# Kernel tuning notes

Hardware: AMD Instinct MI355X
Metric: run time of the kernel (lower is better)

Reference implementation:

```python
import jax, jax.numpy as jnp
import numpy as np

D_IN = 32
D_MODEL = 128
B, T = 512, 512
INPUT_DIM = 2 * D_IN  # concat_mask=True, d_u=0


def setup_inputs() -> dict:
    key = jax.random.key(0)
    ks = jax.random.split(key, 8)
    scale = 0.05
    return {
        "x": jax.random.normal(ks[0], (B, T, D_IN), dtype=jnp.float32),
        "W_ih": jax.random.normal(ks[1], (3 * D_MODEL, INPUT_DIM), dtype=jnp.float32) * scale,
        "W_hh": jax.random.normal(ks[2], (3 * D_MODEL, D_MODEL), dtype=jnp.float32) * scale,
        "b_ih": jax.random.normal(ks[3], (3 * D_MODEL,), dtype=jnp.float32) * scale,
        "b_hh": jax.random.normal(ks[4], (3 * D_MODEL,), dtype=jnp.float32) * scale,
        "W_out": jax.random.normal(ks[5], (D_IN, D_MODEL), dtype=jnp.float32) * scale,
        "b_out": jax.random.normal(ks[6], (D_IN,), dtype=jnp.float32) * scale,
        "mask": jax.random.randint(ks[7], (B, T, D_IN), 0, 2, dtype=jnp.int32),
    }


def reference(x, W_ih, W_hh, b_ih, b_hh, W_out, b_out, mask):
    m_bool = mask.astype(bool)                      # [B,T,d_in]
    m_f = mask.astype(x.dtype)
    x = jnp.where(m_bool, x, jnp.zeros_like(x))     # zero-fill missing

    h0 = jnp.zeros((x.shape[0], D_MODEL), dtype=x.dtype)   # state_init='zero'
    x_hat0 = h0 @ W_out.T + b_out                   # readout of initial state

    def gru_cell(x_t, h):
        gx = x_t @ W_ih.T + b_ih                    # [B, 3*d_model]
        gh = h @ W_hh.T + b_hh
        xr, xz, xn = jnp.split(gx, 3, axis=-1)
        hr, hz, hn = jnp.split(gh, 3, axis=-1)
        r = jax.nn.sigmoid(xr + hr)
        z = jax.nn.sigmoid(xz + hz)
        n = jnp.tanh(xn + r * hn)
        return (1.0 - z) * n + z * h

    def step(carry, inp):
        h, x_hat = carry
        x_s, mb_s, mf_s = inp                       # [B,d_in] each
        x_p = jnp.where(mb_s, x_s, x_hat)           # fill blanks with prediction
        x_t = jnp.concatenate([x_p, mf_s], axis=-1) # concat_mask=True
        h_new = gru_cell(x_t, h)
        x_hat_new = h_new @ W_out.T + b_out
        return (h_new, x_hat_new), x_hat_new

    # scan over steps 0..T-2 (time-major)
    xs = jnp.swapaxes(x[:, :-1], 0, 1)              # [T-1, B, d_in]
    mbs = jnp.swapaxes(m_bool[:, :-1], 0, 1)
    mfs = jnp.swapaxes(m_f[:, :-1], 0, 1)
    _, preds = jax.lax.scan(step, (h0, x_hat0), (xs, mbs, mfs))  # [T-1, B, d_in]

    out = jnp.concatenate([x_hat0[None], preds], axis=0)         # [T, B, d_in]
    return jnp.swapaxes(out, 0, 1)                                # [B, T, d_in]
```

## Files before the change

### kernel.cpp

```cpp
#include <hip/hip_runtime.h>
#include <hip/hip_bf16.h>

#define D_IN 32
#define TT 512
#define GB 16
#define NBLK 32
#define MAGIC 0x51F7C0DEu

typedef __attribute__((ext_vector_type(8))) short bf16x8;
typedef __attribute__((ext_vector_type(4))) float f32x4;
typedef __attribute__((ext_vector_type(4))) int   i32x4;
typedef __attribute__((ext_vector_type(2))) unsigned u32x2;

__device__ inline short bf16_of(float f) {
    union { float f; unsigned u; } v; v.f = f;
    unsigned r = v.u + 0x7FFFu + ((v.u >> 16) & 1u);
    return (short)(r >> 16);
}
__device__ inline unsigned pack2(float a, float b) {
    return ((unsigned)(unsigned short)bf16_of(a)) |
           (((unsigned)(unsigned short)bf16_of(b)) << 16);
}
__device__ inline bf16x8 load8_bf16(const float* __restrict__ p) {
    bf16x8 r;
#pragma unroll
    for (int e = 0; e < 8; ++e) r[e] = bf16_of(p[e]);
    return r;
}
__device__ inline f32x4 splat4(float v) { return (f32x4){v, v, v, v}; }

__device__ inline float sigmoid_fast(float x) {
    return __builtin_amdgcn_rcpf(1.0f + __expf(-x));
}
__device__ inline float tanh_fast(float x) {
    return 1.0f - 2.0f * __builtin_amdgcn_rcpf(__expf(2.0f * x) + 1.0f);
}
__device__ inline void lds_barrier() {
    asm volatile("s_waitcnt lgkmcnt(0)\n\ts_barrier" ::: "memory");
}

__global__ __launch_bounds__(512, 2)
void rnn_imputer(const float* __restrict__ x,
                 const float* __restrict__ W_ih,
                 const float* __restrict__ W_hh,
                 const float* __restrict__ b_ih,
                 const float* __restrict__ b_hh,
                 const float* __restrict__ W_out,
                 const float* __restrict__ b_out,
                 const int*   __restrict__ mask,
                 float* __restrict__ out,
                 unsigned*    flags,
                 int          use_spin) {
    if (blockIdx.x >= NBLK) {
        if (!use_spin || threadIdx.x >= 64) return;
        const unsigned long long t0 = __builtin_amdgcn_s_memrealtime();
        float a0 = 1.0f + threadIdx.x * 1e-6f, a1 = a0 + 0.1f, a2 = a0 + 0.2f,
              a3 = a0 + 0.3f, a4 = a0 + 0.4f, a5 = a0 + 0.5f, a6 = a0 + 0.6f,
              a7 = a0 + 0.7f;
        for (;;) {
            unsigned acc = 0;
#pragma unroll
            for (int j = 0; j < NBLK; ++j)
                acc |= (__hip_atomic_load(&flags[j], __ATOMIC_RELAXED,
                                          __HIP_MEMORY_SCOPE_AGENT) ^ MAGIC);
            if (acc == 0) break;
            if (__builtin_amdgcn_s_memrealtime() - t0 > 200000ull) break;
            for (int i = 0; i < 32; ++i) {
                a0 = __builtin_fmaf(a0, 1.0000001f, 1e-8f);
                a1 = __builtin_fmaf(a1, 1.0000001f, 1e-8f);
                a2 = __builtin_fmaf(a2, 1.0000001f, 1e-8f);
                a3 = __builtin_fmaf(a3, 1.0000001f, 1e-8f);
                a4 = __builtin_fmaf(a4, 1.0000001f, 1e-8f);
                a5 = __builtin_fmaf(a5, 1.0000001f, 1e-8f);
                a6 = __builtin_fmaf(a6, 1.0000001f, 1e-8f);
                a7 = __builtin_fmaf(a7, 1.0000001f, 1e-8f);
            }
            __builtin_amdgcn_s_sleep(24);
        }
        const float s = a0 + a1 + a2 + a3 + a4 + a5 + a6 + a7;
        if (s == 1.2345e30f) ((float*)flags)[NBLK + 1] = s;
        return;
    }

    __shared__ __align__(16) float xch[16][GB][36];
    __shared__ __align__(16) int   mch[16][GB][36];
    __shared__ __align__(16) short xt_w[8][GB][40];
    __shared__ __align__(16) short hbuf[2][GB][136];

    const int tid  = threadIdx.x;
    const int wv   = tid >> 6;
    const int lane = tid & 63;
    const int q    = lane >> 4;
    const int c    = lane & 15;
    const int bb   = blockIdx.x * GB;
    const int brow = bb + c;
    const int i_col = wv * 16 + c;

    bf16x8 Br[6], Bz[6], Bxn[2], Bhn[4];
#pragma unroll
    for (int kt = 0; kt < 6; ++kt) {
        const int k = kt * 32 + q * 8;
        const float* sr = (k < 64) ? (W_ih + (size_t)i_col * 64 + k)
                                   : (W_hh + (size_t)i_col * 128 + (k - 64));
        Br[kt] = load8_bf16(sr);
        const float* sz = (k < 64) ? (W_ih + (size_t)(128 + i_col) * 64 + k)
                                   : (W_hh + (size_t)(128 + i_col) * 128 + (k - 64));
        Bz[kt] = load8_bf16(sz);
    }
#pragma unroll
    for (int kt = 0; kt < 2; ++kt)
        Bxn[kt] = load8_bf16(W_ih + (size_t)(256 + i_col) * 64 + kt * 32 + q * 8);
#pragma unroll
    for (int kt = 0; kt < 4; ++kt)
        Bhn[kt] = load8_bf16(W_hh + (size_t)(256 + i_col) * 128 + kt * 32 + q * 8);

    bf16x8 Ao[2][4];
#pragma unroll
    for (int ta = 0; ta < 2; ++ta)
#pragma unroll
        for (int kt = 0; kt < 4; ++kt)
            Ao[ta][kt] = load8_bf16(W_out + (size_t)(ta * 16 + c) * 128 + kt * 32 + q * 8);

    f32x4 bo_v[2];
#pragma unroll
    for (int ta = 0; ta < 2; ++ta)
        bo_v[ta] = *(const f32x4*)&b_out[ta * 16 + q * 4];

    const float bR  = b_ih[i_col]       + b_hh[i_col];
    const float bZ  = b_ih[128 + i_col] + b_hh[128 + i_col];
    const float bXN = b_ih[256 + i_col];
    const float bHN = b_hh[256 + i_col];

    float h_reg[4] = {0.f, 0.f, 0.f, 0.f};

    bf16x8 A0, A1;
    {
        const size_t o = (size_t)brow * TT * D_IN + q * 8;
        const f32x4 xa = *(const f32x4*)&x[o];
        const f32x4 xb = *(const f32x4*)&x[o + 4];
        const i32x4 ma = *(const i32x4*)&mask[o];
        const i32x4 mb = *(const i32x4*)&mask[o + 4];
        union { bf16x8 v; unsigned d[4]; } a0, a1;
#pragma unroll
        for (int j = 0; j < 4; ++j) {
            const float fa = ma[j] ? xa[j] : b_out[q * 8 + j];
            const float fb = mb[j] ? xb[j] : b_out[q * 8 + 4 + j];
            ((short*)&a0.v)[j]     = bf16_of(fa);
            ((short*)&a0.v)[4 + j] = bf16_of(fb);
            ((short*)&a1.v)[j]     = ma[j] ? (short)0x3F80 : (short)0;
            ((short*)&a1.v)[4 + j] = mb[j] ? (short)0x3F80 : (short)0;
        }
        A0 = a0.v; A1 = a1.v;
    }
#pragma unroll
    for (int ta = 0; ta < 2; ++ta)
        if (wv == ta)
            *(f32x4*)&out[(size_t)brow * TT * D_IN + ta * 16 + q * 4] = bo_v[ta];

#pragma unroll
    for (int rnd = 0; rnd < 4; ++rnd) {
        const int ts  = 1 + rnd * 4 + (tid >> 7);
        const int row = (tid >> 3) & 15;
        const int c4  = (tid & 7) * 4;
        const size_t o = ((size_t)(bb + row) * TT + ts) * D_IN + c4;
        *(f32x4*)&xch[ts & 15][row][c4] = *(const f32x4*)&x[o];
        *(i32x4*)&mch[ts & 15][row][c4] = *(const i32x4*)&mask[o];
    }

    f32x4 Ra = __builtin_amdgcn_mfma_f32_16x16x32_bf16(A1, Br[1],  splat4(bR), 0, 0, 0);
    f32x4 Za = __builtin_amdgcn_mfma_f32_16x16x32_bf16(A1, Bz[1],  splat4(bZ), 0, 0, 0);
    f32x4 XN = __builtin_amdgcn_mfma_f32_16x16x32_bf16(A1, Bxn[1], splat4(bXN), 0, 0, 0);
    f32x4 Rb = splat4(0.f), Zb = splat4(0.f);
    f32x4 HN = splat4(bHN);

    __syncthreads();

    for (int t = 0; t < TT - 1; ++t) {
        Rb = __builtin_amdgcn_mfma_f32_16x16x32_bf16(A0, Br[0],  Rb, 0, 0, 0);
        Zb = __builtin_amdgcn_mfma_f32_16x16x32_bf16(A0, Bz[0],  Zb, 0, 0, 0);
        XN = __builtin_amdgcn_mfma_f32_16x16x32_bf16(A0, Bxn[0], XN, 0, 0, 0);

        const int sl = (t + 1) & 15;
        const f32x4 pfx0 = *(const f32x4*)&xch[sl][c][q * 4];
        const f32x4 pfx1 = *(const f32x4*)&xch[sl][c][16 + q * 4];
        const i32x4 pfm0 = *(const i32x4*)&mch[sl][c][q * 4];
        const i32x4 pfm1 = *(const i32x4*)&mch[sl][c][16 + q * 4];
        const i32x4 pfa0 = *(const i32x4*)&mch[sl][c][q * 8];
        const i32x4 pfa1 = *(const i32x4*)&mch[sl][c][q * 8 + 4];

        const int pb = (t + 1) & 1;
#pragma unroll
        for (int r = 0; r < 4; ++r) {
            const float rr = sigmoid_fast(Ra[r] + Rb[r]);
            const float zz = sigmoid_fast(Za[r] + Zb[r]);
            const float nn = tanh_fast(XN[r] + rr * HN[r]);
            const float h  = nn + zz * (h_reg[r] - nn);
            h_reg[r] = h;
            hbuf[pb][q * 4 + r][i_col] = bf16_of(h);
        }

        if ((t & 7) == 7) {
#pragma unroll
            for (int rnd = 0; rnd < 2; ++rnd) {
                const int tsu = t + 9 + rnd * 4 + (tid >> 7);
                const int ts  = tsu <= TT - 1 ? tsu : TT - 1;
                const int row = (tid >> 3) & 15;
                const int c4  = (tid & 7) * 4;
                const size_t o = ((size_t)(bb + row) * TT + ts) * D_IN + c4;
                *(f32x4*)&xch[tsu & 15][row][c4] = *(const f32x4*)&x[o];
                *(i32x4*)&mch[tsu & 15][row][c4] = *(const i32x4*)&mask[o];
            }
        }
        lds_barrier();

        bf16x8 Ah[4];
#pragma unroll
        for (int kt = 0; kt < 4; ++kt)
            Ah[kt] = *(const bf16x8*)&hbuf[pb][c][kt * 32 + q * 8];

        f32x4 aO0a = __builtin_amdgcn_mfma_f32_16x16x32_bf16(Ao[0][0], Ah[0], bo_v[0], 0, 0, 0);
        f32x4 aO1a = __builtin_amdgcn_mfma_f32_16x16x32_bf16(Ao[1][0], Ah[0], bo_v[1], 0, 0, 0);
        f32x4 aO0b = __builtin_amdgcn_mfma_f32_16x16x32_bf16(Ao[0][2], Ah[2], splat4(0.f), 0, 0, 0);
        f32x4 aO1b = __builtin_amdgcn_mfma_f32_16x16x32_bf16(Ao[1][2], Ah[2], splat4(0.f), 0, 0, 0);
        aO0a = __builtin_amdgcn_mfma_f32_16x16x32_bf16(Ao[0][1], Ah[1], aO0a, 0, 0, 0);
        aO1a = __builtin_amdgcn_mfma_f32_16x16x32_bf16(Ao[1][1], Ah[1], aO1a, 0, 0, 0);
        aO0b = __builtin_amdgcn_mfma_f32_16x16x32_bf16(Ao[0][3], Ah[3], aO0b, 0, 0, 0);
        aO1b = __builtin_amdgcn_mfma_f32_16x16x32_bf16(Ao[1][3], Ah[3], aO1b, 0, 0, 0);

        Ra = __builtin_amdgcn_mfma_f32_16x16x32_bf16(Ah[0], Br[2], splat4(bR), 0, 0, 0);
        Za = __builtin_amdgcn_mfma_f32_16x16x32_bf16(Ah[0], Bz[2], splat4(bZ), 0, 0, 0);
        HN = __builtin_amdgcn_mfma_f32_16x16x32_bf16(Ah[0], Bhn[0], splat4(bHN), 0, 0, 0);
        Rb = __builtin_amdgcn_mfma_f32_16x16x32_bf16(Ah[2], Br[4], splat4(0.f), 0, 0, 0);
        Zb = __builtin_amdgcn_mfma_f32_16x16x32_bf16(Ah[2], Bz[4], splat4(0.f), 0, 0, 0);
        Ra = __builtin_amdgcn_mfma_f32_16x16x32_bf16(Ah[1], Br[3], Ra, 0, 0, 0);
        Za = __builtin_amdgcn_mfma_f32_16x16x32_bf16(Ah[1], Bz[3], Za, 0, 0, 0);
        HN = __builtin_amdgcn_mfma_f32_16x16x32_bf16(Ah[1], Bhn[1], HN, 0, 0, 0);
        Rb = __builtin_amdgcn_mfma_f32_16x16x32_bf16(Ah[3], Br[5], Rb, 0, 0, 0);
        Zb = __builtin_amdgcn_mfma_f32_16x16x32_bf16(Ah[3], Bz[5], Zb, 0, 0, 0);
        HN = __builtin_amdgcn_mfma_f32_16x16x32_bf16(Ah[2], Bhn[2], HN, 0, 0, 0);
        HN = __builtin_amdgcn_mfma_f32_16x16x32_bf16(Ah[3], Bhn[3], HN, 0, 0, 0);

        {
            union { bf16x8 v; unsigned d[4]; } a1;
            a1.d[0] = (pfa0[0] ? 0x3F80u : 0u) | ((pfa0[1] ? 0x3F80u : 0u) << 16);
            a1.d[1] = (pfa0[2] ? 0x3F80u : 0u) | ((pfa0[3] ? 0x3F80u : 0u) << 16);
            a1.d[2] = (pfa1[0] ? 0x3F80u : 0u) | ((pfa1[1] ? 0x3F80u : 0u) << 16);
            a1.d[3] = (pfa1[2] ? 0x3F80u : 0u) | ((pfa1[3] ? 0x3F80u : 0u) << 16);
            A1 = a1.v;
        }
        Ra = __builtin_amdgcn_mfma_f32_16x16x32_bf16(A1, Br[1],  Ra, 0, 0, 0);
        Za = __builtin_amdgcn_mfma_f32_16x16x32_bf16(A1, Bz[1],  Za, 0, 0, 0);
        XN = __builtin_amdgcn_mfma_f32_16x16x32_bf16(A1, Bxn[1], splat4(bXN), 0, 0, 0);

#pragma unroll
        for (int ta = 0; ta < 2; ++ta) {
            f32x4 xh;
            const f32x4 a = ta ? aO1a : aO0a;
            const f32x4 b = ta ? aO1b : aO0b;
#pragma unroll
            for (int r = 0; r < 4; ++r) xh[r] = a[r] + b[r];
            if (wv == ta)
                *(f32x4*)&out[((size_t)brow * TT + (t + 1)) * D_IN + ta * 16 + q * 4] = xh;
            const f32x4 fx = ta ? pfx1 : pfx0;
            const i32x4 fm = ta ? pfm1 : pfm0;
            const float v0 = fm[0] ? fx[0] : xh[0];
            const float v1 = fm[1] ? fx[1] : xh[1];
            const float v2 = fm[2] ? fx[2] : xh[2];
            const float v3 = fm[3] ? fx[3] : xh[3];
            u32x2 px;
            px[0] = pack2(v0, v1);
            px[1] = pack2(v2, v3);
            *(u32x2*)&xt_w[wv][c][ta * 16 + q * 4] = px;
        }
        A0 = *(const bf16x8*)&xt_w[wv][c][q * 8];
    }

    if (use_spin && tid == 0)
        __hip_atomic_store(&flags[blockIdx.x], MAGIC, __ATOMIC_RELAXED,
                           __HIP_MEMORY_SCOPE_AGENT);
}

extern "C" void kernel_launch(void* const* d_in, const int* in_sizes, int n_in,
                              void* d_out, int out_size, void* d_ws, size_t ws_size,
                              hipStream_t stream) {
    const float* x     = (const float*)d_in[0];
    const float* W_ih  = (const float*)d_in[1];
    const float* W_hh  = (const float*)d_in[2];
    const float* b_ih  = (const float*)d_in[3];
    const float* b_hh  = (const float*)d_in[4];
    const float* W_out = (const float*)d_in[5];
    const float* b_out = (const float*)d_in[6];
    const int*   mask  = (const int*)d_in[7];
    float* out = (float*)d_out;

    const int use_spin = (d_ws != nullptr && ws_size >= 256) ? 1 : 0;
    const int grid = use_spin ? 256 : NBLK;

    rnn_imputer<<<dim3(grid), dim3(512), 0, stream>>>(
        x, W_ih, W_hh, b_ih, b_hh, W_out, b_out, mask, out,
        (unsigned*)d_ws, use_spin);
}
```

Baseline: 676.0 us.

## Permute input K layout to build A0 in registers, drop LDS round-trip

Reorders the input-weight K dimension so each lane's MFMA A-operand for the input matches the x_hat/x columns it already holds, which removes the per-step LDS store/load through xt_w and the extra mask reads. The bf16 packing now uses the v_cvt_pk_bf16_f32 instruction. Global prefetch loads are staged in registers and written to LDS a step later, so load latency no longer stalls inside the step. The HN accumulation is split into two independent MFMA chains to shorten the dependency chain. The cost is more live registers and reliance on the permuted layout being consistent across all weight, x and mask loads.

After: 666.1 us. No clear change (-1.5%).

```diff
diff --git a/kernel.cpp b/kernel.cpp
--- a/kernel.cpp
+++ b/kernel.cpp
@@ -10,21 +10,30 @@
 typedef __attribute__((ext_vector_type(8))) short bf16x8;
 typedef __attribute__((ext_vector_type(4))) float f32x4;
 typedef __attribute__((ext_vector_type(4))) int   i32x4;
-typedef __attribute__((ext_vector_type(2))) unsigned u32x2;
 
 __device__ inline short bf16_of(float f) {
     union { float f; unsigned u; } v; v.f = f;
     unsigned r = v.u + 0x7FFFu + ((v.u >> 16) & 1u);
     return (short)(r >> 16);
 }
-__device__ inline unsigned pack2(float a, float b) {
-    return ((unsigned)(unsigned short)bf16_of(a)) |
-           (((unsigned)(unsigned short)bf16_of(b)) << 16);
+__device__ inline unsigned cvt_pk_bf16(float lo, float hi) {
+    unsigned r;
+    asm("v_cvt_pk_bf16_f32 %0, %1, %2" : "=v"(r) : "v"(lo), "v"(hi));
+    return r;
 }
 __device__ inline bf16x8 load8_bf16(const float* __restrict__ p) {
     bf16x8 r;
 #pragma unroll
     for (int e = 0; e < 8; ++e) r[e] = bf16_of(p[e]);
+    return r;
+}
+__device__ inline bf16x8 load44_bf16(const float* __restrict__ p, int qq) {
+    bf16x8 r;
+#pragma unroll
+    for (int e = 0; e < 4; ++e) {
+        r[e]     = bf16_of(p[qq * 4 + e]);
+        r[4 + e] = bf16_of(p[16 + qq * 4 + e]);
+    }
     return r;
 }
 __device__ inline f32x4 splat4(float v) { return (f32x4){v, v, v, v}; }
@@ -84,7 +93,6 @@
 
     __shared__ __align__(16) float xch[16][GB][36];
     __shared__ __align__(16) int   mch[16][GB][36];
-    __shared__ __align__(16) short xt_w[8][GB][40];
     __shared__ __align__(16) short hbuf[2][GB][136];
 
     const int tid  = threadIdx.x;
@@ -97,19 +105,18 @@
     const int i_col = wv * 16 + c;
 
     bf16x8 Br[6], Bz[6], Bxn[2], Bhn[4];
-#pragma unroll
-    for (int kt = 0; kt < 6; ++kt) {
-        const int k = kt * 32 + q * 8;
-        const float* sr = (k < 64) ? (W_ih + (size_t)i_col * 64 + k)
-                                   : (W_hh + (size_t)i_col * 128 + (k - 64));
-        Br[kt] = load8_bf16(sr);
-        const float* sz = (k < 64) ? (W_ih + (size_t)(128 + i_col) * 64 + k)
-                                   : (W_hh + (size_t)(128 + i_col) * 128 + (k - 64));
-        Bz[kt] = load8_bf16(sz);
-    }
-#pragma unroll
-    for (int kt = 0; kt < 2; ++kt)
-        Bxn[kt] = load8_bf16(W_ih + (size_t)(256 + i_col) * 64 + kt * 32 + q * 8);
+    Br[0]  = load44_bf16(W_ih + (size_t)i_col * 64, q);
+    Br[1]  = load44_bf16(W_ih + (size_t)i_col * 64 + 32, q);
+    Bz[0]  = load44_bf16(W_ih + (size_t)(128 + i_col) * 64, q);
+    Bz[1]  = load44_bf16(W_ih + (size_t)(128 + i_col) * 64 + 32, q);
+    Bxn[0] = load44_bf16(W_ih + (size_t)(256 + i_col) * 64, q);
+    Bxn[1] = load44_bf16(W_ih + (size_t)(256 + i_col) * 64 + 32, q);
+#pragma unroll
+    for (int kt = 2; kt < 6; ++kt) {
+        const int k = (kt - 2) * 32 + q * 8;
+        Br[kt] = load8_bf16(W_hh + (size_t)i_col * 128 + k);
+        Bz[kt] = load8_bf16(W_hh + (size_t)(128 + i_col) * 128 + k);
+    }
 #pragma unroll
     for (int kt = 0; kt < 4; ++kt)
         Bhn[kt] = load8_bf16(W_hh + (size_t)(256 + i_col) * 128 + kt * 32 + q * 8);
@@ -135,16 +142,16 @@
 
     bf16x8 A0, A1;
     {
-        const size_t o = (size_t)brow * TT * D_IN + q * 8;
-        const f32x4 xa = *(const f32x4*)&x[o];
-        const f32x4 xb = *(const f32x4*)&x[o + 4];
-        const i32x4 ma = *(const i32x4*)&mask[o];
-        const i32x4 mb = *(const i32x4*)&mask[o + 4];
+        const size_t o = (size_t)brow * TT * D_IN;
+        const f32x4 xa = *(const f32x4*)&x[o + q * 4];
+        const f32x4 xb = *(const f32x4*)&x[o + 16 + q * 4];
+        const i32x4 ma = *(const i32x4*)&mask[o + q * 4];
+        const i32x4 mb = *(const i32x4*)&mask[o + 16 + q * 4];
         union { bf16x8 v; unsigned d[4]; } a0, a1;
 #pragma unroll
         for (int j = 0; j < 4; ++j) {
-            const float fa = ma[j] ? xa[j] : b_out[q * 8 + j];
-            const float fb = mb[j] ? xb[j] : b_out[q * 8 + 4 + j];
+            const float fa = ma[j] ? xa[j] : b_out[q * 4 + j];
+            const float fb = mb[j] ? xb[j] : b_out[16 + q * 4 + j];
             ((short*)&a0.v)[j]     = bf16_of(fa);
             ((short*)&a0.v)[4 + j] = bf16_of(fb);
             ((short*)&a1.v)[j]     = ma[j] ? (short)0x3F80 : (short)0;
@@ -171,7 +178,10 @@
     f32x4 Za = __builtin_amdgcn_mfma_f32_16x16x32_bf16(A1, Bz[1],  splat4(bZ), 0, 0, 0);
     f32x4 XN = __builtin_amdgcn_mfma_f32_16x16x32_bf16(A1, Bxn[1], splat4(bXN), 0, 0, 0);
     f32x4 Rb = splat4(0.f), Zb = splat4(0.f);
-    f32x4 HN = splat4(bHN);
+    f32x4 HNa = splat4(bHN), HNb = splat4(0.f);
+
+    f32x4 sgx[2] = {splat4(0.f), splat4(0.f)};
+    i32x4 sgm[2] = {(i32x4){0,0,0,0}, (i32x4){0,0,0,0}};
 
     __syncthreads();
 
@@ -185,20 +195,17 @@
         const f32x4 pfx1 = *(const f32x4*)&xch[sl][c][16 + q * 4];
         const i32x4 pfm0 = *(const i32x4*)&mch[sl][c][q * 4];
         const i32x4 pfm1 = *(const i32x4*)&mch[sl][c][16 + q * 4];
-        const i32x4 pfa0 = *(const i32x4*)&mch[sl][c][q * 8];
-        const i32x4 pfa1 = *(const i32x4*)&mch[sl][c][q * 8 + 4];
-
-        const int pb = (t + 1) & 1;
-#pragma unroll
-        for (int r = 0; r < 4; ++r) {
-            const float rr = sigmoid_fast(Ra[r] + Rb[r]);
-            const float zz = sigmoid_fast(Za[r] + Zb[r]);
-            const float nn = tanh_fast(XN[r] + rr * HN[r]);
-            const float h  = nn + zz * (h_reg[r] - nn);
-            h_reg[r] = h;
-            hbuf[pb][q * 4 + r][i_col] = bf16_of(h);
-        }
-
+
+        if ((t & 7) == 0 && t) {
+#pragma unroll
+            for (int rnd = 0; rnd < 2; ++rnd) {
+                const int tsu = t + 8 + rnd * 4 + (tid >> 7);
+                const int row = (tid >> 3) & 15;
+                const int c4  = (tid & 7) * 4;
+                *(f32x4*)&xch[tsu & 15][row][c4] = sgx[rnd];
+                *(i32x4*)&mch[tsu & 15][row][c4] = sgm[rnd];
+            }
+        }
         if ((t & 7) == 7) {
 #pragma unroll
             for (int rnd = 0; rnd < 2; ++rnd) {
@@ -207,10 +214,22 @@
                 const int row = (tid >> 3) & 15;
                 const int c4  = (tid & 7) * 4;
                 const size_t o = ((size_t)(bb + row) * TT + ts) * D_IN + c4;
-                *(f32x4*)&xch[tsu & 15][row][c4] = *(const f32x4*)&x[o];
-                *(i32x4*)&mch[tsu & 15][row][c4] = *(const i32x4*)&mask[o];
+                sgx[rnd] = *(const f32x4*)&x[o];
+                sgm[rnd] = *(const i32x4*)&mask[o];
             }
         }
+
+        const int pb = (t + 1) & 1;
+#pragma unroll
+        for (int r = 0; r < 4; ++r) {
+            const float rr = sigmoid_fast(Ra[r] + Rb[r]);
+            const float zz = sigmoid_fast(Za[r] + Zb[r]);
+            const float nn = tanh_fast(XN[r] + rr * (HNa[r] + HNb[r]));
+            const float h  = nn + zz * (h_reg[r] - nn);
+            h_reg[r] = h;
+            hbuf[pb][q * 4 + r][i_col] = bf16_of(h);
+        }
+
         lds_barrier();
 
         bf16x8 Ah[4];
@@ -227,52 +246,58 @@
         aO0b = __builtin_amdgcn_mfma_f32_16x16x32_bf16(Ao[0][3], Ah[3], aO0b, 0, 0, 0);
         aO1b = __builtin_amdgcn_mfma_f32_16x16x32_bf16(Ao[1][3], Ah[3], aO1b, 0, 0, 0);
 
-        Ra = __builtin_amdgcn_mfma_f32_16x16x32_bf16(Ah[0], Br[2], splat4(bR), 0, 0, 0);
-        Za = __builtin_amdgcn_mfma_f32_16x16x32_bf16(Ah[0], Bz[2], splat4(bZ), 0, 0, 0);
-        HN = __builtin_amdgcn_mfma_f32_16x16x32_bf16(Ah[0], Bhn[0], splat4(bHN), 0, 0, 0);
-        Rb = __builtin_amdgcn_mfma_f32_16x16x32_bf16(Ah[2], Br[4], splat4(0.f), 0, 0, 0);
-        Zb = __builtin_amdgcn_mfma_f32_16x16x32_bf16(Ah[2], Bz[4], splat4(0.f), 0, 0, 0);
-        Ra = __builtin_amdgcn_mfma_f32_16x16x32_bf16(Ah[1], Br[3], Ra, 0, 0, 0);
-        Za = __builtin_amdgcn_mfma_f32_16x16x32_bf16(Ah[1], Bz[3], Za, 0, 0, 0);
-        HN = __builtin_amdgcn_mfma_f32_16x16x32_bf16(Ah[1], Bhn[1], HN, 0, 0, 0);
-        Rb = __builtin_amdgcn_mfma_f32_16x16x32_bf16(Ah[3], Br[5], Rb, 0, 0, 0);
-        Zb = __builtin_amdgcn_mfma_f32_16x16x32_bf16(Ah[3], Bz[5], Zb, 0, 0, 0);
-        HN = __builtin_amdgcn_mfma_f32_16x16x32_bf16(Ah[2], Bhn[2], HN, 0, 0, 0);
-        HN = __builtin_amdgcn_mfma_f32_16x16x32_bf16(Ah[3], Bhn[3], HN, 0, 0, 0);
+        Ra  = __builtin_amdgcn_mfma_f32_16x16x32_bf16(Ah[0], Br[2], splat4(bR), 0, 0, 0);
+        Za  = __builtin_amdgcn_mfma_f32_16x16x32_bf16(Ah[0], Bz[2], splat4(bZ), 0, 0, 0);
+        HNa = __builtin_amdgcn_mfma_f32_16x16x32_bf16(Ah[0], Bhn[0], splat4(bHN), 0, 0, 0);
+        Rb  = __builtin_amdgcn_mfma_f32_16x16x32_bf16(Ah[2], Br[4], splat4(0.f), 0, 0, 0);
+        Zb  = __builtin_amdgcn_mfma_f32_16x16x32_bf16(Ah[2], Bz[4], splat4(0.f), 0, 0, 0);
+        Ra  = __builtin_amdgcn_mfma_f32_16x16x32_bf16(Ah[1], Br[3], Ra, 0, 0, 0);
+        Za  = __builtin_amdgcn_mfma_f32_16x16x32_bf16(Ah[1], Bz[3], Za, 0, 0, 0);
+        HNa = __builtin_amdgcn_mfma_f32_16x16x32_bf16(Ah[1], Bhn[1], HNa, 0, 0, 0);
+        Rb  = __builtin_amdgcn_mfma_f32_16x16x32_bf16(Ah[3], Br[5], Rb, 0, 0, 0);
+        Zb  = __builtin_amdgcn_mfma_f32_16x16x32_bf16(Ah[3], Bz[5], Zb, 0, 0, 0);
+        HNb = __builtin_amdgcn_mfma_f32_16x16x32_bf16(Ah[2], Bhn[2], splat4(0.f), 0, 0, 0);
+        HNb = __builtin_amdgcn_mfma_f32_16x16x32_bf16(Ah[3], Bhn[3], HNb, 0, 0, 0);
 
         {
             union { bf16x8 v; unsigned d[4]; } a1;
-            a1.d[0] = (pfa0[0] ? 0x3F80u : 0u) | ((pfa0[1] ? 0x3F80u : 0u) << 16);
-            a1.d[1] = (pfa0[2] ? 0x3F80u : 0u) | ((pfa0[3] ? 0x3F80u : 0u) << 16);
-            a1.d[2] = (pfa1[0] ? 0x3F80u : 0u) | ((pfa1[1] ? 0x3F80u : 0u) << 16);
-            a1.d[3] = (pfa1[2] ? 0x3F80u : 0u) | ((pfa1[3] ? 0x3F80u : 0u) << 16);
+            a1.d[0] = (pfm0[0] ? 0x3F80u : 0u) | ((pfm0[1] ? 0x3F80u : 0u) << 16);
+            a1.d[1] = (pfm0[2] ? 0x3F80u : 0u) | ((pfm0[3] ? 0x3F80u : 0u) << 16);
+            a1.d[2] = (pfm1[0] ? 0x3F80u : 0u) | ((pfm1[1] ? 0x3F80u : 0u) << 16);
+            a1.d[3] = (pfm1[2] ? 0x3F80u : 0u) | ((pfm1[3] ? 0x3F80u : 0u) << 16);
             A1 = a1.v;
         }
         Ra = __builtin_amdgcn_mfma_f32_16x16x32_bf16(A1, Br[1],  Ra, 0, 0, 0);
         Za = __builtin_amdgcn_mfma_f32_16x16x32_bf16(A1, Bz[1],  Za, 0, 0, 0);
         XN = __builtin_amdgcn_mfma_f32_16x16x32_bf16(A1, Bxn[1], splat4(bXN), 0, 0, 0);
 
-#pragma unroll
-        for (int ta = 0; ta < 2; ++ta) {
-            f32x4 xh;
-            const f32x4 a = ta ? aO1a : aO0a;
-            const f32x4 b = ta ? aO1b : aO0b;
-#pragma unroll
-            for (int r = 0; r < 4; ++r) xh[r] = a[r] + b[r];
-            if (wv == ta)
-                *(f32x4*)&out[((size_t)brow * TT + (t + 1)) * D_IN + ta * 16 + q * 4] = xh;
-            const f32x4 fx = ta ? pfx1 : pfx0;
-            const i32x4 fm = ta ? pfm1 : pfm0;
-            const float v0 = fm[0] ? fx[0] : xh[0];
-            const float v1 = fm[1] ? fx[1] : xh[1];
-            const float v2 = fm[2] ? fx[2] : xh[2];
-            const float v3 = fm[3] ? fx[3] : xh[3];
-            u32x2 px;
-            px[0] = pack2(v0, v1);
-            px[1] = pack2(v2, v3);
-            *(u32x2*)&xt_w[wv][c][ta * 16 + q * 4] = px;
-        }
-        A0 = *(const bf16x8*)&xt_w[wv][c][q * 8];
+        {
+            f32x4 xh0, xh1;
+#pragma unroll
+            for (int r = 0; r < 4; ++r) {
+                xh0[r] = aO0a[r] + aO0b[r];
+                xh1[r] = aO1a[r] + aO1b[r];
+            }
+            if (wv == 0)
+                *(f32x4*)&out[((size_t)brow * TT + (t + 1)) * D_IN + q * 4] = xh0;
+            if (wv == 1)
+                *(f32x4*)&out[((size_t)brow * TT + (t + 1)) * D_IN + 16 + q * 4] = xh1;
+
+            const float v00 = pfm0[0] ? pfx0[0] : xh0[0];
+            const float v01 = pfm0[1] ? pfx0[1] : xh0[1];
+            const float v02 = pfm0[2] ? pfx0[2] : xh0[2];
+            const float v03 = pfm0[3] ? pfx0[3] : xh0[3];
+            const float v10 = pfm1[0] ? pfx1[0] : xh1[0];
+            const float v11 = pfm1[1] ? pfx1[1] : xh1[1];
+            const float v12 = pfm1[2] ? pfx1[2] : xh1[2];
+            const float v13 = pfm1[3] ? pfx1[3] : xh1[3];
+            union { bf16x8 v; unsigned d[4]; } a0;
+            a0.d[0] = cvt_pk_bf16(v00, v01);
+            a0.d[1] = cvt_pk_bf16(v02, v03);
+            a0.d[2] = cvt_pk_bf16(v10, v11);
+            a0.d[3] = cvt_pk_bf16(v12, v13);
+            A0 = a0.v;
+        }
     }
 
     if (use_spin && tid == 0)
```
